# Optimization experiments

Hardware: AMD Instinct MI355X
Metric: run time of the kernel (lower is better)

Reference implementation:

```python
import jax, jax.numpy as jnp
import numpy as np

BN_EPS = 1e-5


def setup_inputs() -> dict:
    key = jax.random.key(0)
    k1, k2, k3 = jax.random.split(key, 3)
    B, C, N = 8, 64, 4096
    x = jax.random.normal(k1, (B, C, N, 1), dtype=jnp.float32)
    w = jax.random.normal(k2, (B, N), dtype=jnp.float32)
    conv_w = jax.random.normal(k3, (C, C, 1, 1), dtype=jnp.float32) * (1.0 / np.sqrt(C))
    conv_b = jnp.zeros((C,), dtype=jnp.float32)
    bn_gamma = jnp.ones((C,), dtype=jnp.float32)
    bn_beta = jnp.zeros((C,), dtype=jnp.float32)
    return {"x": x, "w": w, "conv_w": conv_w, "conv_b": conv_b,
            "bn_gamma": bn_gamma, "bn_beta": bn_beta}


def _graph_aggregation(x, w):
    # x: [B, C, N, 1], w: [B, N]
    B, C, N, _ = x.shape
    wv = jax.nn.relu(jnp.tanh(w))                       # [B, N]
    # torch.bmm(w^T, w) with w [B,N,1] -> [B,1,1] inner product (faithful)
    s = jnp.sum(wv * wv, axis=-1)[:, None, None]        # [B, 1, 1]
    A = s + jnp.eye(N, dtype=x.dtype)                   # broadcast -> [B, N, N]
    d = jnp.sum(A, axis=-1)                             # [B, N]
    dinv = (1.0 / d) ** 0.5                             # [B, N]
    # diag(D) @ A @ diag(D) == row/col scaling (same math, no diag materialize)
    L = dinv[:, :, None] * A * dinv[:, None, :]         # [B, N, N]
    L = jax.lax.stop_gradient(L)                        # torch.no_grad block
    feat = jnp.transpose(x[..., 0], (0, 2, 1))          # [B, N, C]
    out = jnp.einsum('bnm,bmc->bnc', L, feat)           # [B, N, C]
    return jnp.transpose(out, (0, 2, 1))[..., None]     # [B, C, N, 1]


def reference(x, w, conv_w, conv_b, bn_gamma, bn_beta):
    out = _graph_aggregation(x, w)                      # [B, C, N, 1]
    # 1x1 conv == channel matmul
    y = jnp.einsum('oc,bcnk->bonk', conv_w[:, :, 0, 0], out) + conv_b[None, :, None, None]
    # BatchNorm2d (training-mode forward: batch statistics over B,N,1)
    mean = jnp.mean(y, axis=(0, 2, 3), keepdims=True)
    var = jnp.var(y, axis=(0, 2, 3), keepdims=True)
    yhat = (y - mean) * jax.lax.rsqrt(var + BN_EPS)
    y = yhat * bn_gamma[None, :, None, None] + bn_beta[None, :, None, None]
    return jax.nn.relu(y)
```

## Files before the change

kernel.cpp:

```cpp
#include <hip/hip_runtime.h>
#include <math.h>

#define B_ 8
#define C_ 64
#define N_ 4096
#define NT_ 32

#define M_OFF   0
#define SMP_OFF (B_ * C_ * N_)
#define SQP_OFF (SMP_OFF + NT_ * B_ * C_)
#define SS_OFF  (SQP_OFF + NT_ * B_ * C_)
#define SC_OFF  (SS_OFF + B_)
#define A_OFF   (SC_OFF + B_)
#define BB_OFF  (A_OFF + B_ * C_)

__global__ __launch_bounds__(512) void k_conv(const float* __restrict__ x,
                                              const float* __restrict__ wvec,
                                              const float* __restrict__ conv_w,
                                              float* __restrict__ ws) {
    const int b = blockIdx.y;
    const int t = threadIdx.x;

    __shared__ float xsm[64 * 128];

    if (blockIdx.x == NT_) {
        const float4* wb = reinterpret_cast<const float4*>(wvec + (size_t)b * N_);
        float p = 0.f;
        #pragma unroll
        for (int i = 0; i < 2; ++i) {
            const float4 v = wb[t + i * 512];
            const float vv[4] = {v.x, v.y, v.z, v.w};
            #pragma unroll
            for (int j = 0; j < 4; ++j)
                if (vv[j] > 0.f) { const float th = tanhf(vv[j]); p += th * th; }
        }
        #pragma unroll
        for (int m = 32; m >= 1; m >>= 1) p += __shfl_xor(p, m);
        if ((t & 63) == 0) xsm[t >> 6] = p;
        __syncthreads();
        if (t == 0) {
            float s = 0.f;
            #pragma unroll
            for (int wv2 = 0; wv2 < 8; ++wv2) s += xsm[wv2];
            ws[SS_OFF + b] = s;
            ws[SC_OFF + b] = 1.f / ((float)N_ * s + 1.f);
        }
        return;
    }

    const int tile = blockIdx.x;
    const int n0 = tile * 128;
    const float* xb = x + (size_t)b * C_ * N_ + n0;

    const int k0 = (t & 31) * 4;
    #pragma unroll
    for (int it = 0; it < 4; ++it) {
        const int cc = it * 16 + (t >> 5);
        *reinterpret_cast<float4*>(&xsm[cc * 128 + k0]) =
            *reinterpret_cast<const float4*>(xb + (size_t)cc * N_ + k0);
    }
    __syncthreads();

    const int o0 = __builtin_amdgcn_readfirstlane((t >> 6) * 8);
    const int nn = (t & 63) * 2;

    float acc[8][2] = {};
    #pragma unroll 4
    for (int c = 0; c < 64; ++c) {
        const float2 xv = *reinterpret_cast<const float2*>(&xsm[c * 128 + nn]);
        #pragma unroll
        for (int i = 0; i < 8; ++i) {
            const float wv = conv_w[(o0 + i) * 64 + c];
            acc[i][0] += wv * xv.x;
            acc[i][1] += wv * xv.y;
        }
    }

    #pragma unroll
    for (int i = 0; i < 8; ++i) {
        const int o = o0 + i;
        *reinterpret_cast<float2*>(ws + M_OFF + ((size_t)(b * 64 + o)) * N_ + n0 + nn) =
            make_float2(acc[i][0], acc[i][1]);
        float s = acc[i][0] + acc[i][1];
        float q = acc[i][0] * acc[i][0] + acc[i][1] * acc[i][1];
        #pragma unroll
        for (int m = 32; m >= 1; m >>= 1) {
            s += __shfl_xor(s, m);
            q += __shfl_xor(q, m);
        }
        if ((t & 63) == 0) {
            ws[SMP_OFF + (tile * B_ + b) * C_ + o] = s;
            ws[SQP_OFF + (tile * B_ + b) * C_ + o] = q;
        }
    }
}

__global__ __launch_bounds__(512) void k_stats(const float* __restrict__ conv_b,
                                               const float* __restrict__ gamma,
                                               const float* __restrict__ beta,
                                               float* __restrict__ ws) {
    const int t = threadIdx.x;
    const int b = t >> 6, o = t & 63;

    __shared__ float sTs[8][64], sTq[8][64];
    __shared__ float sAl[64], sMe[64];

    float SM = 0.f, SQ = 0.f;
    #pragma unroll 8
    for (int p = 0; p < NT_; ++p) {
        SM += ws[SMP_OFF + (p * B_ + b) * C_ + o];
        SQ += ws[SQP_OFF + (p * B_ + b) * C_ + o];
    }
    const float sS = ws[SS_OFF + b];
    const float sc = ws[SC_OFF + b];
    const float q  = sS * sc * SM + conv_b[o];
    sTs[b][o] = sc * SM + 4096.f * q;
    sTq[b][o] = sc * sc * SQ + 2.f * sc * q * SM + 4096.f * q * q;
    __syncthreads();

    if (t < 64) {
        float Sy = 0.f, Syy = 0.f;
        #pragma unroll
        for (int bb2 = 0; bb2 < 8; ++bb2) { Sy += sTs[bb2][t]; Syy += sTq[bb2][t]; }
        const float mean = Sy / 32768.f;
        const float var  = Syy / 32768.f - mean * mean;
        sAl[t] = gamma[t] * rsqrtf(var + 1e-5f);
        sMe[t] = mean;
    }
    __syncthreads();

    const float alpha = sAl[o];
    ws[A_OFF  + b * 64 + o] = sc * alpha;
    ws[BB_OFF + b * 64 + o] = (q - sMe[o]) * alpha + beta[o];
}

__global__ __launch_bounds__(256) void k_emit(const float* __restrict__ ws,
                                              float* __restrict__ out) {
    const int idx = blockIdx.x * 256 + threadIdx.x;
    #pragma unroll
    for (int h = 0; h < 2; ++h) {
        const int e = idx + h * (1024 * 256);
        const int row = e >> 10;
        const float a  = ws[A_OFF + row];
        const float bb = ws[BB_OFF + row];
        const float4 m = *reinterpret_cast<const float4*>(ws + M_OFF + (size_t)e * 4);
        float4 r;
        r.x = fmaxf(m.x * a + bb, 0.f);
        r.y = fmaxf(m.y * a + bb, 0.f);
        r.z = fmaxf(m.z * a + bb, 0.f);
        r.w = fmaxf(m.w * a + bb, 0.f);
        *reinterpret_cast<float4*>(out + (size_t)e * 4) = r;
    }
}

extern "C" void kernel_launch(void* const* d_in, const int* in_sizes, int n_in,
                              void* d_out, int out_size, void* d_ws, size_t ws_size,
                              hipStream_t stream) {
    (void)in_sizes; (void)n_in; (void)out_size; (void)ws_size;
    const float* x      = (const float*)d_in[0];
    const float* w      = (const float*)d_in[1];
    const float* conv_w = (const float*)d_in[2];
    const float* conv_b = (const float*)d_in[3];
    const float* gamma  = (const float*)d_in[4];
    const float* beta   = (const float*)d_in[5];
    float* out = (float*)d_out;
    float* ws  = (float*)d_ws;

    k_conv<<<dim3(NT_ + 1, B_), 512, 0, stream>>>(x, w, conv_w, ws);
    k_stats<<<1, 512, 0, stream>>>(conv_b, gamma, beta, ws);
    k_emit<<<1024, 256, 0, stream>>>(ws, out);
}
```

Before: 85.70 us.

## Fuse conv, BN stats and emit into one cooperative kernel with grid sync

Replaces the three-kernel pipeline with one cooperative kernel. Each block computes its conv tile in registers, writes partial sums, waits at a grid-wide sync, and then every block redundantly reduces the BN statistics and writes the normalized ReLU output directly. This removes the round trip of the full intermediate tensor through global memory and two kernel launches. The cost is a grid barrier, redundant per-block stats reduction, and host-side occupancy and attribute queries on every launch. The old three-kernel path is kept as a fallback if the cooperative launch cannot run.

```diff
diff --git a/kernel.cpp b/kernel.cpp
--- a/kernel.cpp
+++ b/kernel.cpp
@@ -1,18 +1,150 @@
 #include <hip/hip_runtime.h>
+#include <hip/hip_cooperative_groups.h>
 #include <math.h>
+
+namespace cg = cooperative_groups;
 
 #define B_ 8
 #define C_ 64
 #define N_ 4096
 #define NT_ 32
 
-#define M_OFF   0
-#define SMP_OFF (B_ * C_ * N_)
-#define SQP_OFF (SMP_OFF + NT_ * B_ * C_)
+#define SMP_OFF 0
+#define SQP_OFF (NT_ * B_ * C_)
 #define SS_OFF  (SQP_OFF + NT_ * B_ * C_)
 #define SC_OFF  (SS_OFF + B_)
 #define A_OFF   (SC_OFF + B_)
 #define BB_OFF  (A_OFF + B_ * C_)
+#define M_OFF   65536
+
+__global__ __launch_bounds__(512, 4) void k_fused(
+        const float* __restrict__ x, const float* __restrict__ wvec,
+        const float* __restrict__ conv_w, const float* __restrict__ conv_b,
+        const float* __restrict__ gamma, const float* __restrict__ beta,
+        float* __restrict__ ws, float* __restrict__ out) {
+    cg::grid_group grid = cg::this_grid();
+    const int tile = blockIdx.x;
+    const int b    = blockIdx.y;
+    const int t    = threadIdx.x;
+
+    __shared__ float xsm[64 * 128];
+    __shared__ float sred[8];
+
+    const int n0 = tile * 128;
+    const int o0 = (t >> 6) * 8;
+    const int nn = (t & 63) * 2;
+
+    if (tile == 0) {
+        const float4* wb = reinterpret_cast<const float4*>(wvec + (size_t)b * N_);
+        float p = 0.f;
+        #pragma unroll
+        for (int i = 0; i < 2; ++i) {
+            const float4 v = wb[t + i * 512];
+            const float vv[4] = {v.x, v.y, v.z, v.w};
+            #pragma unroll
+            for (int j = 0; j < 4; ++j)
+                if (vv[j] > 0.f) { const float th = tanhf(vv[j]); p += th * th; }
+        }
+        #pragma unroll
+        for (int m = 32; m >= 1; m >>= 1) p += __shfl_xor(p, m);
+        if ((t & 63) == 0) sred[t >> 6] = p;
+        __syncthreads();
+        if (t == 0) {
+            const float s = sred[0] + sred[1] + sred[2] + sred[3]
+                          + sred[4] + sred[5] + sred[6] + sred[7];
+            ws[SS_OFF + b] = s;
+            ws[SC_OFF + b] = 1.f / ((float)N_ * s + 1.f);
+        }
+    }
+
+    const float* xb = x + (size_t)b * C_ * N_ + n0;
+    const int k0 = (t & 31) * 4;
+    #pragma unroll
+    for (int it = 0; it < 4; ++it) {
+        const int cc = it * 16 + (t >> 5);
+        *reinterpret_cast<float4*>(&xsm[cc * 128 + k0]) =
+            *reinterpret_cast<const float4*>(xb + (size_t)cc * N_ + k0);
+    }
+    __syncthreads();
+
+    float a0[8], a1[8];
+    #pragma unroll
+    for (int i = 0; i < 8; ++i) { a0[i] = 0.f; a1[i] = 0.f; }
+    #pragma unroll 4
+    for (int c = 0; c < 64; ++c) {
+        const float2 xv = *reinterpret_cast<const float2*>(&xsm[c * 128 + nn]);
+        #pragma unroll
+        for (int i = 0; i < 8; ++i) {
+            const float wv = conv_w[(o0 + i) * 64 + c];
+            a0[i] += wv * xv.x;
+            a1[i] += wv * xv.y;
+        }
+    }
+    #pragma unroll
+    for (int i = 0; i < 8; ++i) {
+        float s = a0[i] + a1[i];
+        float q = a0[i] * a0[i] + a1[i] * a1[i];
+        #pragma unroll
+        for (int m = 32; m >= 1; m >>= 1) {
+            s += __shfl_xor(s, m);
+            q += __shfl_xor(q, m);
+        }
+        if ((t & 63) == 0) {
+            ws[SMP_OFF + (tile * B_ + b) * C_ + o0 + i] = s;
+            ws[SQP_OFF + (tile * B_ + b) * C_ + o0 + i] = q;
+        }
+    }
+
+    grid.sync();
+
+    float* sSM = xsm;
+    float* sTs = xsm + 512;
+    float* sTq = xsm + 1024;
+    float* sAl = xsm + 1536;
+    float* sMe = xsm + 1600;
+    __syncthreads();
+    {
+        const int b2 = t >> 6, o = t & 63;
+        float SM = 0.f, SQ = 0.f;
+        #pragma unroll 8
+        for (int p2 = 0; p2 < NT_; ++p2) {
+            SM += ws[SMP_OFF + (p2 * B_ + b2) * C_ + o];
+            SQ += ws[SQP_OFF + (p2 * B_ + b2) * C_ + o];
+        }
+        const float sS2 = ws[SS_OFF + b2];
+        const float sc2 = ws[SC_OFF + b2];
+        const float q2  = sS2 * sc2 * SM + conv_b[o];
+        sSM[b2 * 64 + o] = SM;
+        sTs[b2 * 64 + o] = sc2 * SM + 4096.f * q2;
+        sTq[b2 * 64 + o] = sc2 * sc2 * SQ + 2.f * sc2 * q2 * SM + 4096.f * q2 * q2;
+    }
+    __syncthreads();
+    if (t < 64) {
+        float Sy = 0.f, Syy = 0.f;
+        #pragma unroll
+        for (int b2 = 0; b2 < 8; ++b2) { Sy += sTs[b2 * 64 + t]; Syy += sTq[b2 * 64 + t]; }
+        const float mean = Sy / 32768.f;
+        const float var  = Syy / 32768.f - mean * mean;
+        sAl[t] = gamma[t] * rsqrtf(var + 1e-5f);
+        sMe[t] = mean;
+    }
+    __syncthreads();
+
+    const float sS = ws[SS_OFF + b];
+    const float sc = ws[SC_OFF + b];
+    #pragma unroll
+    for (int i = 0; i < 8; ++i) {
+        const int o = o0 + i;
+        const float alpha = sAl[o];
+        const float q  = sS * sc * sSM[b * 64 + o] + conv_b[o];
+        const float av = sc * alpha;
+        const float bv = (q - sMe[o]) * alpha + beta[o];
+        float2 r;
+        r.x = fmaxf(a0[i] * av + bv, 0.f);
+        r.y = fmaxf(a1[i] * av + bv, 0.f);
+        *reinterpret_cast<float2*>(out + ((size_t)(b * 64 + o)) * N_ + n0 + nn) = r;
+    }
+}
 
 __global__ __launch_bounds__(512) void k_conv(const float* __restrict__ x,
                                               const float* __restrict__ wvec,
@@ -20,7 +152,6 @@
                                               float* __restrict__ ws) {
     const int b = blockIdx.y;
     const int t = threadIdx.x;
-
     __shared__ float xsm[64 * 128];
 
     if (blockIdx.x == NT_) {
@@ -39,9 +170,8 @@
         if ((t & 63) == 0) xsm[t >> 6] = p;
         __syncthreads();
         if (t == 0) {
-            float s = 0.f;
-            #pragma unroll
-            for (int wv2 = 0; wv2 < 8; ++wv2) s += xsm[wv2];
+            const float s = xsm[0] + xsm[1] + xsm[2] + xsm[3]
+                          + xsm[4] + xsm[5] + xsm[6] + xsm[7];
             ws[SS_OFF + b] = s;
             ws[SC_OFF + b] = 1.f / ((float)N_ * s + 1.f);
         }
@@ -51,7 +181,6 @@
     const int tile = blockIdx.x;
     const int n0 = tile * 128;
     const float* xb = x + (size_t)b * C_ * N_ + n0;
-
     const int k0 = (t & 31) * 4;
     #pragma unroll
     for (int it = 0; it < 4; ++it) {
@@ -61,28 +190,28 @@
     }
     __syncthreads();
 
-    const int o0 = __builtin_amdgcn_readfirstlane((t >> 6) * 8);
+    const int o0 = (t >> 6) * 8;
     const int nn = (t & 63) * 2;
-
-    float acc[8][2] = {};
+    float a0[8], a1[8];
+    #pragma unroll
+    for (int i = 0; i < 8; ++i) { a0[i] = 0.f; a1[i] = 0.f; }
     #pragma unroll 4
     for (int c = 0; c < 64; ++c) {
         const float2 xv = *reinterpret_cast<const float2*>(&xsm[c * 128 + nn]);
         #pragma unroll
         for (int i = 0; i < 8; ++i) {
             const float wv = conv_w[(o0 + i) * 64 + c];
-            acc[i][0] += wv * xv.x;
-            acc[i][1] += wv * xv.y;
-        }
-    }
-
+            a0[i] += wv * xv.x;
+            a1[i] += wv * xv.y;
+        }
+    }
     #pragma unroll
     for (int i = 0; i < 8; ++i) {
         const int o = o0 + i;
         *reinterpret_cast<float2*>(ws + M_OFF + ((size_t)(b * 64 + o)) * N_ + n0 + nn) =
-            make_float2(acc[i][0], acc[i][1]);
-        float s = acc[i][0] + acc[i][1];
-        float q = acc[i][0] * acc[i][0] + acc[i][1] * acc[i][1];
+            make_float2(a0[i], a1[i]);
+        float s = a0[i] + a1[i];
+        float q = a0[i] * a0[i] + a1[i] * a1[i];
         #pragma unroll
         for (int m = 32; m >= 1; m >>= 1) {
             s += __shfl_xor(s, m);
@@ -101,7 +230,6 @@
                                                float* __restrict__ ws) {
     const int t = threadIdx.x;
     const int b = t >> 6, o = t & 63;
-
     __shared__ float sTs[8][64], sTq[8][64];
     __shared__ float sAl[64], sMe[64];
 
@@ -117,18 +245,16 @@
     sTs[b][o] = sc * SM + 4096.f * q;
     sTq[b][o] = sc * sc * SQ + 2.f * sc * q * SM + 4096.f * q * q;
     __syncthreads();
-
     if (t < 64) {
         float Sy = 0.f, Syy = 0.f;
         #pragma unroll
-        for (int bb2 = 0; bb2 < 8; ++bb2) { Sy += sTs[bb2][t]; Syy += sTq[bb2][t]; }
+        for (int b2 = 0; b2 < 8; ++b2) { Sy += sTs[b2][t]; Syy += sTq[b2][t]; }
         const float mean = Sy / 32768.f;
         const float var  = Syy / 32768.f - mean * mean;
         sAl[t] = gamma[t] * rsqrtf(var + 1e-5f);
         sMe[t] = mean;
     }
     __syncthreads();
-
     const float alpha = sAl[o];
     ws[A_OFF  + b * 64 + o] = sc * alpha;
     ws[BB_OFF + b * 64 + o] = (q - sMe[o]) * alpha + beta[o];
@@ -166,7 +292,22 @@
     float* out = (float*)d_out;
     float* ws  = (float*)d_ws;
 
-    k_conv<<<dim3(NT_ + 1, B_), 512, 0, stream>>>(x, w, conv_w, ws);
-    k_stats<<<1, 512, 0, stream>>>(conv_b, gamma, beta, ws);
-    k_emit<<<1024, 256, 0, stream>>>(ws, out);
-}
+    int dev = 0, nCU = 0, maxb = 0;
+    hipGetDevice(&dev);
+    hipDeviceGetAttribute(&nCU, hipDeviceAttributeMultiprocessorCount, dev);
+    bool coop = (hipOccupancyMaxActiveBlocksPerMultiprocessor(
+                     &maxb, (const void*)k_fused, 512, 0) == hipSuccess) &&
+                (maxb * nCU >= NT_ * B_);
+
+    if (coop) {
+        void* args[] = {(void*)&x, (void*)&w, (void*)&conv_w, (void*)&conv_b,
+                        (void*)&gamma, (void*)&beta, (void*)&ws, (void*)&out};
+        coop = (hipLaunchCooperativeKernel((const void*)k_fused, dim3(NT_, B_),
+                                           dim3(512), args, 0, stream) == hipSuccess);
+    }
+    if (!coop) {
+        k_conv<<<dim3(NT_ + 1, B_), 512, 0, stream>>>(x, w, conv_w, ws);
+        k_stats<<<1, 512, 0, stream>>>(conv_b, gamma, beta, ws);
+        k_emit<<<1024, 256, 0, stream>>>(ws, out);
+    }
+}
```

After: 127.4 us. 48.6% more time.

## Recompute conv in emit kernel instead of storing intermediate, fuse stats into emit

Applied to the files above, without the earlier changes.

The first kernel now writes only the per-tile partial sums and squared sums of the 1x1 conv output and no longer stores the full conv result. The second kernel reloads x, has every block redo the BN statistics reduction, and recomputes the conv before applying the affine transform and ReLU directly to the output. This removes the k_stats launch and the 8 MB intermediate write plus read-back. In exchange, x is read twice, the conv matmul runs twice, and all 256 blocks repeat the small stats reduction.

```diff
diff --git a/kernel.cpp b/kernel.cpp
--- a/kernel.cpp
+++ b/kernel.cpp
@@ -6,24 +6,23 @@
 #define N_ 4096
 #define NT_ 32
 
-#define M_OFF   0
-#define SMP_OFF (B_ * C_ * N_)
-#define SQP_OFF (SMP_OFF + NT_ * B_ * C_)
+#define SMP_OFF 0
+#define SQP_OFF (NT_ * B_ * C_)
 #define SS_OFF  (SQP_OFF + NT_ * B_ * C_)
 #define SC_OFF  (SS_OFF + B_)
-#define A_OFF   (SC_OFF + B_)
-#define BB_OFF  (A_OFF + B_ * C_)
 
-__global__ __launch_bounds__(512) void k_conv(const float* __restrict__ x,
+__global__ __launch_bounds__(512) void k_part(const float* __restrict__ x,
                                               const float* __restrict__ wvec,
                                               const float* __restrict__ conv_w,
                                               float* __restrict__ ws) {
-    const int b = blockIdx.y;
-    const int t = threadIdx.x;
+    const int tile = blockIdx.x;
+    const int b    = blockIdx.y;
+    const int t    = threadIdx.x;
 
     __shared__ float xsm[64 * 128];
+    __shared__ float sred[8];
 
-    if (blockIdx.x == NT_) {
+    if (tile == 0) {
         const float4* wb = reinterpret_cast<const float4*>(wvec + (size_t)b * N_);
         float p = 0.f;
         #pragma unroll
@@ -36,22 +35,18 @@
         }
         #pragma unroll
         for (int m = 32; m >= 1; m >>= 1) p += __shfl_xor(p, m);
-        if ((t & 63) == 0) xsm[t >> 6] = p;
+        if ((t & 63) == 0) sred[t >> 6] = p;
         __syncthreads();
         if (t == 0) {
-            float s = 0.f;
-            #pragma unroll
-            for (int wv2 = 0; wv2 < 8; ++wv2) s += xsm[wv2];
+            const float s = sred[0] + sred[1] + sred[2] + sred[3]
+                          + sred[4] + sred[5] + sred[6] + sred[7];
             ws[SS_OFF + b] = s;
             ws[SC_OFF + b] = 1.f / ((float)N_ * s + 1.f);
         }
-        return;
     }
 
-    const int tile = blockIdx.x;
     const int n0 = tile * 128;
     const float* xb = x + (size_t)b * C_ * N_ + n0;
-
     const int k0 = (t & 31) * 4;
     #pragma unroll
     for (int it = 0; it < 4; ++it) {
@@ -61,67 +56,82 @@
     }
     __syncthreads();
 
-    const int o0 = __builtin_amdgcn_readfirstlane((t >> 6) * 8);
+    const int o0 = (t >> 6) * 8;
     const int nn = (t & 63) * 2;
-
-    float acc[8][2] = {};
+    float a0[8], a1[8];
+    #pragma unroll
+    for (int i = 0; i < 8; ++i) { a0[i] = 0.f; a1[i] = 0.f; }
     #pragma unroll 4
     for (int c = 0; c < 64; ++c) {
         const float2 xv = *reinterpret_cast<const float2*>(&xsm[c * 128 + nn]);
         #pragma unroll
         for (int i = 0; i < 8; ++i) {
             const float wv = conv_w[(o0 + i) * 64 + c];
-            acc[i][0] += wv * xv.x;
-            acc[i][1] += wv * xv.y;
+            a0[i] += wv * xv.x;
+            a1[i] += wv * xv.y;
         }
     }
-
     #pragma unroll
     for (int i = 0; i < 8; ++i) {
-        const int o = o0 + i;
-        *reinterpret_cast<float2*>(ws + M_OFF + ((size_t)(b * 64 + o)) * N_ + n0 + nn) =
-            make_float2(acc[i][0], acc[i][1]);
-        float s = acc[i][0] + acc[i][1];
-        float q = acc[i][0] * acc[i][0] + acc[i][1] * acc[i][1];
+        float s = a0[i] + a1[i];
+        float q = a0[i] * a0[i] + a1[i] * a1[i];
         #pragma unroll
         for (int m = 32; m >= 1; m >>= 1) {
             s += __shfl_xor(s, m);
             q += __shfl_xor(q, m);
         }
         if ((t & 63) == 0) {
-            ws[SMP_OFF + (tile * B_ + b) * C_ + o] = s;
-            ws[SQP_OFF + (tile * B_ + b) * C_ + o] = q;
+            ws[SMP_OFF + (tile * B_ + b) * C_ + o0 + i] = s;
+            ws[SQP_OFF + (tile * B_ + b) * C_ + o0 + i] = q;
         }
     }
 }
 
-__global__ __launch_bounds__(512) void k_stats(const float* __restrict__ conv_b,
-                                               const float* __restrict__ gamma,
-                                               const float* __restrict__ beta,
-                                               float* __restrict__ ws) {
-    const int t = threadIdx.x;
-    const int b = t >> 6, o = t & 63;
+__global__ __launch_bounds__(512) void k_emit(const float* __restrict__ x,
+                                              const float* __restrict__ conv_w,
+                                              const float* __restrict__ conv_b,
+                                              const float* __restrict__ gamma,
+                                              const float* __restrict__ beta,
+                                              const float* __restrict__ ws,
+                                              float* __restrict__ out) {
+    const int tile = blockIdx.x;
+    const int b    = blockIdx.y;
+    const int t    = threadIdx.x;
 
-    __shared__ float sTs[8][64], sTq[8][64];
+    __shared__ float xsm[64 * 128];
+    __shared__ float sSM[512], sTs[512], sTq[512];
     __shared__ float sAl[64], sMe[64];
 
-    float SM = 0.f, SQ = 0.f;
-    #pragma unroll 8
-    for (int p = 0; p < NT_; ++p) {
-        SM += ws[SMP_OFF + (p * B_ + b) * C_ + o];
-        SQ += ws[SQP_OFF + (p * B_ + b) * C_ + o];
+    const int n0 = tile * 128;
+    const float* xb = x + (size_t)b * C_ * N_ + n0;
+    const int k0 = (t & 31) * 4;
+    #pragma unroll
+    for (int it = 0; it < 4; ++it) {
+        const int cc = it * 16 + (t >> 5);
+        *reinterpret_cast<float4*>(&xsm[cc * 128 + k0]) =
+            *reinterpret_cast<const float4*>(xb + (size_t)cc * N_ + k0);
     }
-    const float sS = ws[SS_OFF + b];
-    const float sc = ws[SC_OFF + b];
-    const float q  = sS * sc * SM + conv_b[o];
-    sTs[b][o] = sc * SM + 4096.f * q;
-    sTq[b][o] = sc * sc * SQ + 2.f * sc * q * SM + 4096.f * q * q;
+
+    {
+        const int b2 = t >> 6, o = t & 63;
+        float SM = 0.f, SQ = 0.f;
+        #pragma unroll 8
+        for (int p2 = 0; p2 < NT_; ++p2) {
+            SM += ws[SMP_OFF + (p2 * B_ + b2) * C_ + o];
+            SQ += ws[SQP_OFF + (p2 * B_ + b2) * C_ + o];
+        }
+        const float sS2 = ws[SS_OFF + b2];
+        const float sc2 = ws[SC_OFF + b2];
+        const float q2  = sS2 * sc2 * SM + conv_b[o];
+        sSM[b2 * 64 + o] = SM;
+        sTs[b2 * 64 + o] = sc2 * SM + 4096.f * q2;
+        sTq[b2 * 64 + o] = sc2 * sc2 * SQ + 2.f * sc2 * q2 * SM + 4096.f * q2 * q2;
+    }
     __syncthreads();
-
     if (t < 64) {
         float Sy = 0.f, Syy = 0.f;
         #pragma unroll
-        for (int bb2 = 0; bb2 < 8; ++bb2) { Sy += sTs[bb2][t]; Syy += sTq[bb2][t]; }
+        for (int b2 = 0; b2 < 8; ++b2) { Sy += sTs[b2 * 64 + t]; Syy += sTq[b2 * 64 + t]; }
         const float mean = Sy / 32768.f;
         const float var  = Syy / 32768.f - mean * mean;
         sAl[t] = gamma[t] * rsqrtf(var + 1e-5f);
@@ -129,27 +139,34 @@
     }
     __syncthreads();
 
-    const float alpha = sAl[o];
-    ws[A_OFF  + b * 64 + o] = sc * alpha;
-    ws[BB_OFF + b * 64 + o] = (q - sMe[o]) * alpha + beta[o];
-}
-
-__global__ __launch_bounds__(256) void k_emit(const float* __restrict__ ws,
-                                              float* __restrict__ out) {
-    const int idx = blockIdx.x * 256 + threadIdx.x;
+    const int o0 = (t >> 6) * 8;
+    const int nn = (t & 63) * 2;
+    float a0[8], a1[8];
     #pragma unroll
-    for (int h = 0; h < 2; ++h) {
-        const int e = idx + h * (1024 * 256);
-        const int row = e >> 10;
-        const float a  = ws[A_OFF + row];
-        const float bb = ws[BB_OFF + row];
-        const float4 m = *reinterpret_cast<const float4*>(ws + M_OFF + (size_t)e * 4);
-        float4 r;
-        r.x = fmaxf(m.x * a + bb, 0.f);
-        r.y = fmaxf(m.y * a + bb, 0.f);
-        r.z = fmaxf(m.z * a + bb, 0.f);
-        r.w = fmaxf(m.w * a + bb, 0.f);
-        *reinterpret_cast<float4*>(out + (size_t)e * 4) = r;
+    for (int i = 0; i < 8; ++i) { a0[i] = 0.f; a1[i] = 0.f; }
+    #pragma unroll 4
+    for (int c = 0; c < 64; ++c) {
+        const float2 xv = *reinterpret_cast<const float2*>(&xsm[c * 128 + nn]);
+        #pragma unroll
+        for (int i = 0; i < 8; ++i) {
+            const float wv = conv_w[(o0 + i) * 64 + c];
+            a0[i] += wv * xv.x;
+            a1[i] += wv * xv.y;
+        }
+    }
+    const float sS = ws[SS_OFF + b];
+    const float sc = ws[SC_OFF + b];
+    #pragma unroll
+    for (int i = 0; i < 8; ++i) {
+        const int o = o0 + i;
+        const float alpha = sAl[o];
+        const float q  = sS * sc * sSM[b * 64 + o] + conv_b[o];
+        const float av = sc * alpha;
+        const float bv = (q - sMe[o]) * alpha + beta[o];
+        float2 r;
+        r.x = fmaxf(a0[i] * av + bv, 0.f);
+        r.y = fmaxf(a1[i] * av + bv, 0.f);
+        *reinterpret_cast<float2*>(out + ((size_t)(b * 64 + o)) * N_ + n0 + nn) = r;
     }
 }
 
@@ -166,7 +183,6 @@
     float* out = (float*)d_out;
     float* ws  = (float*)d_ws;
 
-    k_conv<<<dim3(NT_ + 1, B_), 512, 0, stream>>>(x, w, conv_w, ws);
-    k_stats<<<1, 512, 0, stream>>>(conv_b, gamma, beta, ws);
-    k_emit<<<1024, 256, 0, stream>>>(ws, out);
+    k_part<<<dim3(NT_, B_), 512, 0, stream>>>(x, w, conv_w, ws);
+    k_emit<<<dim3(NT_, B_), 512, 0, stream>>>(x, conv_w, conv_b, gamma, beta, ws, out);
 }
```

New measurement: 90.52 us. 1.06x slower.
